# Kernel tuning notes

Hardware: AMD Instinct MI355X
Metric: run time of the kernel (lower is better)

The kernel has to match this reference:

```python
import jax, jax.numpy as jnp
import numpy as np
import math

DK = 64  # = in_dim // 4
SCALE = math.sqrt(DK)


def setup_inputs() -> dict:
    key = jax.random.key(0)
    ks = jax.random.split(key, 5)
    B, C, H, W = 8, 256, 64, 64
    x = jax.random.normal(ks[0], (B, C, H, W), dtype=jnp.float32)
    # scale weights down so pre-softmax logits are O(1)
    Wq = jax.random.normal(ks[1], (DK, C), dtype=jnp.float32) * 0.05
    Wk = jax.random.normal(ks[2], (DK, C), dtype=jnp.float32) * 0.05
    Wv = jax.random.normal(ks[3], (C, C), dtype=jnp.float32) * 0.05
    bq = jnp.zeros((DK,), dtype=jnp.float32)
    bk = jnp.zeros((DK,), dtype=jnp.float32)
    bv = jnp.zeros((C,), dtype=jnp.float32)
    gamma = jax.random.normal(ks[4], (1,), dtype=jnp.float32)
    return {"x": x, "Wq": Wq, "bq": bq, "Wk": Wk, "bk": bk,
            "Wv": Wv, "bv": bv, "gamma": gamma}


def reference(x, Wq, bq, Wk, bk, Wv, bv, gamma):
    B, C, H, W = x.shape
    N = H * W
    xf = x.reshape(B, C, N)                                   # [B,C,N]
    # 1x1 convs == per-position linear maps
    q = jnp.einsum('dc,bcn->bnd', Wq, xf) + bq                # [B,N,dk]
    k = jnp.einsum('dc,bcn->bdn', Wk, xf) + bk[:, None]       # [B,dk,N]
    v = jnp.einsum('ec,bcn->ben', Wv, xf) + bv[:, None]       # [B,C,N]
    S = jnp.einsum('bnd,bdm->bnm', q, k) / SCALE              # [B,N,N]
    attn = jax.nn.softmax(S, axis=-1)                         # softmax over keys m
    # torch: bmm(v, attn^T) -> o[b,c,m] = sum_n v[b,c,n] * attn[b,m,n]
    o = jnp.einsum('bcn,bmn->bcm', v, attn).reshape(B, C, H, W)
    return x + gamma[0] * o
```

## Files before the change

### kernel.cpp

```cpp
#include <hip/hip_runtime.h>


typedef __attribute__((ext_vector_type(8)))  short short8;
typedef __attribute__((ext_vector_type(4)))  short short4v;
typedef __attribute__((ext_vector_type(16))) float f32x16;
typedef __attribute__((ext_vector_type(4)))  float f32x4;

#define B_   8
#define C_   256
#define N_   4096
#define DK_  64
#define QSCL 0.18033688011112043f

#if defined(__has_builtin)
#if __has_builtin(__builtin_amdgcn_exp2f)
#define EXP2F(x) __builtin_amdgcn_exp2f(x)
#else
#define EXP2F(x) exp2f(x)
#endif
#else
#define EXP2F(x) exp2f(x)
#endif

__device__ __forceinline__ unsigned short bfb(float f) {
  unsigned u = __builtin_bit_cast(unsigned, f);
  unsigned r = (u + 0x7fffu + ((u >> 16) & 1u)) >> 16;
  return (unsigned short)r;
}

__device__ __forceinline__ unsigned cvtpk(float a, float b) {
  unsigned r;
  asm("v_cvt_pk_bf16_f32 %0, %1, %2" : "=v"(r) : "v"(a), "v"(b));
  return r;
}

__global__ void prep_kernel(const float* __restrict__ Wq, const float* __restrict__ bq,
                            const float* __restrict__ Wk, const float* __restrict__ bk,
                            const float* __restrict__ Wv, const float* __restrict__ bv,
                            unsigned short* __restrict__ Wc, float* __restrict__ biasc) {
  int idx = blockIdx.x * 256 + threadIdx.x;
  if (idx < 384 * 256) {
    int ch = idx >> 8, c = idx & 255;
    float v;
    if (ch < 64)       v = Wq[ch * 256 + c] * QSCL;
    else if (ch < 128) v = Wk[(ch - 64) * 256 + c];
    else               v = Wv[(ch - 128) * 256 + c];
    Wc[idx] = bfb(v);
  }
  if (idx < 384) {
    float bb;
    if (idx < 64)       bb = bq[idx] * QSCL;
    else if (idx < 128) bb = bk[idx - 64];
    else                bb = bv[idx - 128];
    biasc[idx] = bb;
  }
}

__global__ __launch_bounds__(256, 2) void proj_kernel(
    const float* __restrict__ x, const unsigned short* __restrict__ Wc,
    const float* __restrict__ biasc, unsigned short* __restrict__ Qt,
    unsigned short* __restrict__ Kt, unsigned short* __restrict__ V) {
  __shared__ unsigned short XT[64 * 256];
  const int tid = threadIdx.x;
  const int b = blockIdx.y;
  const int n0 = blockIdx.x * 64;

  {
    const f32x4* x4 = (const f32x4*)(x + ((size_t)b * C_) * N_ + n0);
    int c = tid >> 4;
    const int nl = (tid & 15) << 2;
#pragma unroll
    for (int p = 0; p < 16; ++p, c += 16) {
      f32x4 v = x4[(size_t)c * (N_ / 4) + (nl >> 2)];
#pragma unroll
      for (int i = 0; i < 4; ++i) {
        int n = nl + i;
        XT[n * 256 + ((((c >> 3) ^ (n & 15)) << 3) | (c & 7))] = bfb(v[i]);
      }
    }
  }
  __syncthreads();

  const int lane = tid & 63, li = lane & 31, hi = lane >> 5;
  const int w = tid >> 6;
  const int ch0 = 96 * w;

  f32x16 acc[2][3];
#pragma unroll
  for (int mt = 0; mt < 2; ++mt)
#pragma unroll
    for (int j = 0; j < 3; ++j)
#pragma unroll
      for (int r = 0; r < 16; ++r) acc[mt][j][r] = 0.f;

  const short8* Wc8 = (const short8*)Wc;
#pragma unroll
  for (int ks = 0; ks < 16; ++ks) {
    int chunk = 2 * ks + hi;
    short8 a0 = *(const short8*)&XT[(li) * 256 + ((chunk ^ (li & 15)) << 3)];
    short8 a1 = *(const short8*)&XT[(32 + li) * 256 + ((chunk ^ (li & 15)) << 3)];
#pragma unroll
    for (int j = 0; j < 3; ++j) {
      short8 bf = Wc8[(size_t)(ch0 + 32 * j + li) * 32 + chunk];
      acc[0][j] = __builtin_amdgcn_mfma_f32_32x32x16_bf16(a0, bf, acc[0][j], 0, 0, 0);
      acc[1][j] = __builtin_amdgcn_mfma_f32_32x32x16_bf16(a1, bf, acc[1][j], 0, 0, 0);
    }
  }

#pragma unroll
  for (int j = 0; j < 3; ++j) {
    const int chb = ch0 + 32 * j;
    const int ch = chb + li;
    const float bias = biasc[ch];
#pragma unroll
    for (int mt = 0; mt < 2; ++mt) {
      if (chb < 64) {
#pragma unroll
        for (int r = 0; r < 16; ++r) {
          int n = n0 + 32 * mt + (r & 3) + 8 * (r >> 2) + 4 * hi;
          Qt[((size_t)(b * N_ + n) << 6) + ch] = bfb(acc[mt][j][r] + bias);
        }
      } else if (chb < 128) {
#pragma unroll
        for (int r = 0; r < 16; ++r) {
          int n = n0 + 32 * mt + (r & 3) + 8 * (r >> 2) + 4 * hi;
          Kt[((size_t)(b * N_ + n) << 6) + (ch - 64)] = bfb(acc[mt][j][r] + bias);
        }
      } else {
        const int cv = ch - 128;
#pragma unroll
        for (int q = 0; q < 4; ++q) {
          short4v pk;
#pragma unroll
          for (int i = 0; i < 4; ++i) pk[i] = (short)bfb(acc[mt][j][4 * q + i] + bias);
          int n = n0 + 32 * mt + 8 * q + 4 * hi;
          *(short4v*)&V[(size_t)(b * C_ + cv) * N_ + n] = pk;
        }
      }
    }
  }
}

#define PVMFMA(PF0, PF1, PF2, PF3, VF0, VF1, VF2, VF3)                         \
  do {                                                                         \
    __builtin_amdgcn_s_setprio(1);                                             \
    acc16[0][0] = __builtin_amdgcn_mfma_f32_16x16x32_bf16(PF0, VF0, acc16[0][0], 0, 0, 0); \
    acc16[1][0] = __builtin_amdgcn_mfma_f32_16x16x32_bf16(PF1, VF0, acc16[1][0], 0, 0, 0); \
    acc16[2][0] = __builtin_amdgcn_mfma_f32_16x16x32_bf16(PF2, VF0, acc16[2][0], 0, 0, 0); \
    acc16[3][0] = __builtin_amdgcn_mfma_f32_16x16x32_bf16(PF3, VF0, acc16[3][0], 0, 0, 0); \
    acc16[0][1] = __builtin_amdgcn_mfma_f32_16x16x32_bf16(PF0, VF1, acc16[0][1], 0, 0, 0); \
    acc16[1][1] = __builtin_amdgcn_mfma_f32_16x16x32_bf16(PF1, VF1, acc16[1][1], 0, 0, 0); \
    acc16[2][1] = __builtin_amdgcn_mfma_f32_16x16x32_bf16(PF2, VF1, acc16[2][1], 0, 0, 0); \
    acc16[3][1] = __builtin_amdgcn_mfma_f32_16x16x32_bf16(PF3, VF1, acc16[3][1], 0, 0, 0); \
    acc16[0][2] = __builtin_amdgcn_mfma_f32_16x16x32_bf16(PF0, VF2, acc16[0][2], 0, 0, 0); \
    acc16[1][2] = __builtin_amdgcn_mfma_f32_16x16x32_bf16(PF1, VF2, acc16[1][2], 0, 0, 0); \
    acc16[2][2] = __builtin_amdgcn_mfma_f32_16x16x32_bf16(PF2, VF2, acc16[2][2], 0, 0, 0); \
    acc16[3][2] = __builtin_amdgcn_mfma_f32_16x16x32_bf16(PF3, VF2, acc16[3][2], 0, 0, 0); \
    acc16[0][3] = __builtin_amdgcn_mfma_f32_16x16x32_bf16(PF0, VF3, acc16[0][3], 0, 0, 0); \
    acc16[1][3] = __builtin_amdgcn_mfma_f32_16x16x32_bf16(PF1, VF3, acc16[1][3], 0, 0, 0); \
    acc16[2][3] = __builtin_amdgcn_mfma_f32_16x16x32_bf16(PF2, VF3, acc16[2][3], 0, 0, 0); \
    acc16[3][3] = __builtin_amdgcn_mfma_f32_16x16x32_bf16(PF3, VF3, acc16[3][3], 0, 0, 0); \
    __builtin_amdgcn_s_setprio(0);                                             \
  } while (0)

#define FITER(KC0, KC1, KN0, KN1, PB, VB, VN, TN)                              \
  {                                                                            \
    _Pragma("unroll") for (int mt = 0; mt < 4; ++mt) {                         \
      f32x4 st = {0.f, 0.f, 0.f, 0.f};                                         \
      st = __builtin_amdgcn_mfma_f32_16x16x32_bf16(KC0, qb[mt][0], st, 0, 0, 0); \
      st = __builtin_amdgcn_mfma_f32_16x16x32_bf16(KC1, qb[mt][1], st, 0, 0, 0); \
      float e0 = EXP2F(st[0]), e1 = EXP2F(st[1]);                              \
      float e2 = EXP2F(st[2]), e3 = EXP2F(st[3]);                              \
      den[mt] += (e0 + e1) + (e2 + e3);                                        \
      unsigned lo_ = cvtpk(e0, e1), hh_ = cvtpk(e2, e3);                       \
      unsigned long long vv_ =                                                 \
          (unsigned long long)lo_ | ((unsigned long long)hh_ << 32);           \
      *(unsigned long long*)((PB) + 2048 * mt + prow_base + pwoff) = vv_;      \
    }                                                                          \
    __syncthreads();                          \
    KN0 = *(const short8*)(Kp + (size_t)(TN) * 8192);                          \
    KN1 = *(const short8*)(Kp + (size_t)(TN) * 8192 + 64);                     \
    asm volatile("" ::: "memory");      \
    _Pragma("unroll") for (int j = 0; j < 8; ++j)                              \
      __builtin_amdgcn_global_load_lds(                                        \
          (const __attribute__((address_space(1))) unsigned int*)(srcp[j] +    \
                                                                  (size_t)(TN) * 128), \
          (__attribute__((address_space(3))) unsigned int*)((VN) + w * 8192 +  \
                                                            j * 1024),         \
          16, 0, 0);                                                           \
    {                                                                          \
      const char* vwb_ = (VB) + w * 8192 + prow_base;                          \
      const char* pb_ = (PB) + prow_base;                                      \
      short8 pf0 = *(const short8*)(pb_ + off2_0);                             \
      short8 pf1 = *(const short8*)(pb_ + 2048 + off2_0);                      \
      short8 pf2 = *(const short8*)(pb_ + 4096 + off2_0);                      \
      short8 pf3 = *(const short8*)(pb_ + 6144 + off2_0);                      \
      short8 vf0 = *(const short8*)(vwb_ + off2_0);                            \
      short8 vf1 = *(const short8*)(vwb_ + 2048 + off2_0);                     \
      short8 vf2 = *(const short8*)(vwb_ + 4096 + off2_0);                     \
      short8 vf3 = *(const short8*)(vwb_ + 6144 + off2_0);                     \
      PVMFMA(pf0, pf1, pf2, pf3, vf0, vf1, vf2, vf3);                          \
      pf0 = *(const short8*)(pb_ + off2_1);                                    \
      pf1 = *(const short8*)(pb_ + 2048 + off2_1);                             \
      pf2 = *(const short8*)(pb_ + 4096 + off2_1);                             \
      pf3 = *(const short8*)(pb_ + 6144 + off2_1);                             \
      vf0 = *(const short8*)(vwb_ + off2_1);                                   \
      vf1 = *(const short8*)(vwb_ + 2048 + off2_1);                            \
      vf2 = *(const short8*)(vwb_ + 4096 + off2_1);                            \
      vf3 = *(const short8*)(vwb_ + 6144 + off2_1);                            \
      PVMFMA(pf0, pf1, pf2, pf3, vf0, vf1, vf2, vf3);                          \
    }                                                                          \
  }

__global__ __launch_bounds__(256, 2) void flash_kernel(
    const unsigned short* __restrict__ Qt, const unsigned short* __restrict__ Kt,
    const unsigned short* __restrict__ V, const float* __restrict__ x,
    const float* __restrict__ gamma, float* __restrict__ out) {
  __shared__ char SMEM[81920];
  char* VT0 = SMEM;
  char* VT1 = SMEM + 32768;
  char* PT0 = SMEM + 65536;
  char* PT1 = SMEM + 73728;

  const int tid = threadIdx.x;
  const int lane = tid & 63;
  const int lc = lane & 15, lg = lane >> 4;
  const int w = tid >> 6;
  const int id = blockIdx.x;
  const int b = id & 7;
  const int m0 = (id >> 3) << 6;

  short8 qb[4][2];
#pragma unroll
  for (int mt = 0; mt < 4; ++mt)
#pragma unroll
    for (int ks = 0; ks < 2; ++ks)
      qb[mt][ks] = *(const short8*)(Qt + ((size_t)b * N_ + m0 + 16 * mt + lc) * 64 +
                                    32 * ks + 8 * lg);

  f32x4 acc16[4][4];
#pragma unroll
  for (int t16 = 0; t16 < 4; ++t16)
#pragma unroll
    for (int ct = 0; ct < 4; ++ct)
#pragma unroll
      for (int r = 0; r < 4; ++r) acc16[t16][ct][r] = 0.f;
  float den[4] = {0.f, 0.f, 0.f, 0.f};

  const char* Kp = (const char*)Kt + ((size_t)b * N_ + 16 * w + lc) * 128 + 16 * lg;

  const char* vsb = (const char*)V + (size_t)b * C_ * (N_ * 2);
  const char* srcp[8];
#pragma unroll
  for (int j = 0; j < 8; ++j) {
    int L = w * 8192 + j * 1024 + lane * 16;
    int rp = L >> 8, off = L & 255;
    int h = ((off >> 7) ^ (rp >> 2)) & 1;
    int c = 2 * rp + h;
    int kvb = (off ^ ((c & 15) << 4)) & 127;
    srcp[j] = vsb + (size_t)c * (N_ * 2) + kvb;
  }

  const int pkey = lc << 4;
  const int off2_0 = ((((lc & 1) << 7) | (16 * lg))) ^ pkey;
  const int off2_1 = ((((lc & 1) << 7) | 64 | (16 * lg))) ^ pkey;
  const int pwoff = ((((lc & 1) << 7) | (32 * w) | (8 * lg))) ^ pkey;
  const int prow_base = (lc >> 1) * 256;

  short8 kfA0, kfA1, kfB0, kfB1;
  kfA0 = *(const short8*)(Kp);
  kfA1 = *(const short8*)(Kp + 64);
  asm volatile("" ::: "memory");
#pragma unroll
  for (int j = 0; j < 8; ++j)
    __builtin_amdgcn_global_load_lds(
        (const __attribute__((address_space(1))) unsigned int*)(srcp[j]),
        (__attribute__((address_space(3))) unsigned int*)(VT0 + w * 8192 + j * 1024),
        16, 0, 0);

  for (int t = 0; t < 64; t += 2) {
    const int tn1 = t + 1;
    FITER(kfA0, kfA1, kfB0, kfB1, PT0, VT0, VT1, tn1);
    const int tn2 = (t + 2) & 63;
    FITER(kfB0, kfB1, kfA0, kfA1, PT1, VT1, VT0, tn2);
  }

  float* den_lds = (float*)PT0;
#pragma unroll
  for (int mt = 0; mt < 4; ++mt) {
    float d = den[mt];
    d += __shfl_xor(d, 16);
    d += __shfl_xor(d, 32);
    if (lg == 0) den_lds[w * 64 + mt * 16 + lc] = d;
  }
  __syncthreads();

  const float g = gamma[0];
  float ig[4];
#pragma unroll
  for (int mt = 0; mt < 4; ++mt) {
    float dtot = den_lds[0 * 64 + mt * 16 + lc] + den_lds[1 * 64 + mt * 16 + lc] +
                 den_lds[2 * 64 + mt * 16 + lc] + den_lds[3 * 64 + mt * 16 + lc];
    ig[mt] = g / dtot;
  }

#pragma unroll
  for (int t16 = 0; t16 < 4; ++t16) {
    f32x4 idn;
#pragma unroll
    for (int r = 0; r < 4; ++r)
      idn[r] = __shfl(ig[t16], 4 * lg + r);
#pragma unroll
    for (int ct = 0; ct < 4; ++ct) {
      size_t off = ((size_t)b * C_ + 64 * w + 16 * ct + lc) * N_ + m0 + 16 * t16 + 4 * lg;
      f32x4 xv = *(const f32x4*)(x + off);
      f32x4 o;
#pragma unroll
      for (int r = 0; r < 4; ++r) o[r] = xv[r] + idn[r] * acc16[t16][ct][r];
      *(f32x4*)(out + off) = o;
    }
  }
}

extern "C" void kernel_launch(void* const* d_in, const int* in_sizes, int n_in,
                              void* d_out, int out_size, void* d_ws, size_t ws_size,
                              hipStream_t stream) {
  const float* x = (const float*)d_in[0];
  const float* Wq = (const float*)d_in[1];
  const float* bq = (const float*)d_in[2];
  const float* Wk = (const float*)d_in[3];
  const float* bk = (const float*)d_in[4];
  const float* Wv = (const float*)d_in[5];
  const float* bv = (const float*)d_in[6];
  const float* gamma = (const float*)d_in[7];
  float* out = (float*)d_out;

  char* ws = (char*)d_ws;
  unsigned short* Wc = (unsigned short*)(ws);
  float* biasc = (float*)(ws + 196608);
  unsigned short* Qt = (unsigned short*)(ws + 198144);
  unsigned short* Kt = (unsigned short*)(ws + 198144 + 4194304);
  unsigned short* Vv = (unsigned short*)(ws + 198144 + 8388608);

  prep_kernel<<<384, 256, 0, stream>>>(Wq, bq, Wk, bk, Wv, bv, Wc, biasc);
  proj_kernel<<<dim3(64, 8), 256, 0, stream>>>(x, Wc, biasc, Qt, Kt, Vv);
  flash_kernel<<<512, 256, 0, stream>>>(Qt, Kt, Vv, x, gamma, out);
}
```

Before: 136.7 us.

## Software-pipeline QK^T/exp of next tile with PV MFMA of current tile

Restructures the main loop so that each phase computes the scores and exponentials for tile t+1 into the alternate P buffer while issuing the P·V MFMAs for tile t, with one barrier per phase instead of a barrier between the score and PV stages. A prologue computes the first tile's P and K fragments are prefetched two tiles ahead. The aim is to overlap exp/VALU work and LDS stores with matrix-core work and hide barrier latency, at the cost of higher register pressure from holding both fragment sets and more complex buffer indexing.

```diff
diff --git a/kernel.cpp b/kernel.cpp
--- a/kernel.cpp
+++ b/kernel.cpp
@@ -163,53 +163,52 @@
     __builtin_amdgcn_s_setprio(0);                                             \
   } while (0)
 
-#define FITER(KC0, KC1, KN0, KN1, PB, VB, VN, TN)                              \
+#define S_BODY(KS0, KS1, PBW)                                                  \
+  _Pragma("unroll") for (int mt = 0; mt < 4; ++mt) {                           \
+    f32x4 st = {0.f, 0.f, 0.f, 0.f};                                           \
+    st = __builtin_amdgcn_mfma_f32_16x16x32_bf16(KS0, qb[mt][0], st, 0, 0, 0); \
+    st = __builtin_amdgcn_mfma_f32_16x16x32_bf16(KS1, qb[mt][1], st, 0, 0, 0); \
+    float e0 = EXP2F(st[0]), e1 = EXP2F(st[1]);                                \
+    float e2 = EXP2F(st[2]), e3 = EXP2F(st[3]);                                \
+    den[mt] += (e0 + e1) + (e2 + e3);                                          \
+    unsigned lo_ = cvtpk(e0, e1), hh_ = cvtpk(e2, e3);                         \
+    unsigned long long vv_ =                                                   \
+        (unsigned long long)lo_ | ((unsigned long long)hh_ << 32);             \
+    *(unsigned long long*)((PBW) + 2048 * mt + prow_base + pwoff) = vv_;       \
+  }
+
+#define MPHASE(PBR, PBW, VBR, VBW, KS0, KS1, KL0, KL1, TDMA, TK, DO_S)         \
   {                                                                            \
-    _Pragma("unroll") for (int mt = 0; mt < 4; ++mt) {                         \
-      f32x4 st = {0.f, 0.f, 0.f, 0.f};                                         \
-      st = __builtin_amdgcn_mfma_f32_16x16x32_bf16(KC0, qb[mt][0], st, 0, 0, 0); \
-      st = __builtin_amdgcn_mfma_f32_16x16x32_bf16(KC1, qb[mt][1], st, 0, 0, 0); \
-      float e0 = EXP2F(st[0]), e1 = EXP2F(st[1]);                              \
-      float e2 = EXP2F(st[2]), e3 = EXP2F(st[3]);                              \
-      den[mt] += (e0 + e1) + (e2 + e3);                                        \
-      unsigned lo_ = cvtpk(e0, e1), hh_ = cvtpk(e2, e3);                       \
-      unsigned long long vv_ =                                                 \
-          (unsigned long long)lo_ | ((unsigned long long)hh_ << 32);           \
-      *(unsigned long long*)((PB) + 2048 * mt + prow_base + pwoff) = vv_;      \
-    }                                                                          \
-    __syncthreads();                          \
-    KN0 = *(const short8*)(Kp + (size_t)(TN) * 8192);                          \
-    KN1 = *(const short8*)(Kp + (size_t)(TN) * 8192 + 64);                     \
-    asm volatile("" ::: "memory");      \
     _Pragma("unroll") for (int j = 0; j < 8; ++j)                              \
       __builtin_amdgcn_global_load_lds(                                        \
           (const __attribute__((address_space(1))) unsigned int*)(srcp[j] +    \
-                                                                  (size_t)(TN) * 128), \
-          (__attribute__((address_space(3))) unsigned int*)((VN) + w * 8192 +  \
-                                                            j * 1024),         \
-          16, 0, 0);                                                           \
-    {                                                                          \
-      const char* vwb_ = (VB) + w * 8192 + prow_base;                          \
-      const char* pb_ = (PB) + prow_base;                                      \
-      short8 pf0 = *(const short8*)(pb_ + off2_0);                             \
-      short8 pf1 = *(const short8*)(pb_ + 2048 + off2_0);                      \
-      short8 pf2 = *(const short8*)(pb_ + 4096 + off2_0);                      \
-      short8 pf3 = *(const short8*)(pb_ + 6144 + off2_0);                      \
-      short8 vf0 = *(const short8*)(vwb_ + off2_0);                            \
-      short8 vf1 = *(const short8*)(vwb_ + 2048 + off2_0);                     \
-      short8 vf2 = *(const short8*)(vwb_ + 4096 + off2_0);                     \
-      short8 vf3 = *(const short8*)(vwb_ + 6144 + off2_0);                     \
-      PVMFMA(pf0, pf1, pf2, pf3, vf0, vf1, vf2, vf3);                          \
-      pf0 = *(const short8*)(pb_ + off2_1);                                    \
-      pf1 = *(const short8*)(pb_ + 2048 + off2_1);                             \
-      pf2 = *(const short8*)(pb_ + 4096 + off2_1);                             \
-      pf3 = *(const short8*)(pb_ + 6144 + off2_1);                             \
-      vf0 = *(const short8*)(vwb_ + off2_1);                                   \
-      vf1 = *(const short8*)(vwb_ + 2048 + off2_1);                            \
-      vf2 = *(const short8*)(vwb_ + 4096 + off2_1);                            \
-      vf3 = *(const short8*)(vwb_ + 6144 + off2_1);                            \
-      PVMFMA(pf0, pf1, pf2, pf3, vf0, vf1, vf2, vf3);                          \
-    }                                                                          \
+              (size_t)((TDMA) & 63) * 128),                                    \
+          (__attribute__((address_space(3))) unsigned int*)((VBW) + w * 8192 + \
+              j * 1024), 16, 0, 0);                                            \
+    KL0 = *(const short8*)(Kp + (size_t)((TK) & 63) * 8192);                   \
+    KL1 = *(const short8*)(Kp + (size_t)((TK) & 63) * 8192 + 64);              \
+    const char* vwb_ = (VBR) + w * 8192 + prow_base;                           \
+    const char* pb_ = (PBR) + prow_base;                                       \
+    short8 pf0 = *(const short8*)(pb_ + off2_0);                               \
+    short8 pf1 = *(const short8*)(pb_ + 2048 + off2_0);                        \
+    short8 pf2 = *(const short8*)(pb_ + 4096 + off2_0);                        \
+    short8 pf3 = *(const short8*)(pb_ + 6144 + off2_0);                        \
+    short8 vf0 = *(const short8*)(vwb_ + off2_0);                              \
+    short8 vf1 = *(const short8*)(vwb_ + 2048 + off2_0);                       \
+    short8 vf2 = *(const short8*)(vwb_ + 4096 + off2_0);                       \
+    short8 vf3 = *(const short8*)(vwb_ + 6144 + off2_0);                       \
+    if (DO_S) { S_BODY(KS0, KS1, PBW) }                                        \
+    short8 pg0 = *(const short8*)(pb_ + off2_1);                               \
+    short8 pg1 = *(const short8*)(pb_ + 2048 + off2_1);                        \
+    short8 pg2 = *(const short8*)(pb_ + 4096 + off2_1);                        \
+    short8 pg3 = *(const short8*)(pb_ + 6144 + off2_1);                        \
+    short8 vg0 = *(const short8*)(vwb_ + off2_1);                              \
+    short8 vg1 = *(const short8*)(vwb_ + 2048 + off2_1);                       \
+    short8 vg2 = *(const short8*)(vwb_ + 4096 + off2_1);                       \
+    short8 vg3 = *(const short8*)(vwb_ + 6144 + off2_1);                       \
+    PVMFMA(pf0, pf1, pf2, pf3, vf0, vf1, vf2, vf3);                            \
+    PVMFMA(pg0, pg1, pg2, pg3, vg0, vg1, vg2, vg3);                            \
+    __syncthreads();                                                           \
   }
 
 __global__ __launch_bounds__(256, 2) void flash_kernel(
@@ -267,22 +266,26 @@
   const int pwoff = ((((lc & 1) << 7) | (32 * w) | (8 * lg))) ^ pkey;
   const int prow_base = (lc >> 1) * 256;
 
-  short8 kfA0, kfA1, kfB0, kfB1;
-  kfA0 = *(const short8*)(Kp);
-  kfA1 = *(const short8*)(Kp + 64);
-  asm volatile("" ::: "memory");
-#pragma unroll
-  for (int j = 0; j < 8; ++j)
-    __builtin_amdgcn_global_load_lds(
-        (const __attribute__((address_space(1))) unsigned int*)(srcp[j]),
-        (__attribute__((address_space(3))) unsigned int*)(VT0 + w * 8192 + j * 1024),
-        16, 0, 0);
+  short8 kA0, kA1, kB0, kB1;
+  {
+    short8 k00 = *(const short8*)(Kp);
+    short8 k01 = *(const short8*)(Kp + 64);
+    kA0 = *(const short8*)(Kp + 8192);
+    kA1 = *(const short8*)(Kp + 8192 + 64);
+#pragma unroll
+    for (int j = 0; j < 8; ++j)
+      __builtin_amdgcn_global_load_lds(
+          (const __attribute__((address_space(1))) unsigned int*)(srcp[j]),
+          (__attribute__((address_space(3))) unsigned int*)(VT0 + w * 8192 + j * 1024),
+          16, 0, 0);
+    __syncthreads();
+    S_BODY(k00, k01, PT0)
+    __syncthreads();
+  }
 
   for (int t = 0; t < 64; t += 2) {
-    const int tn1 = t + 1;
-    FITER(kfA0, kfA1, kfB0, kfB1, PT0, VT0, VT1, tn1);
-    const int tn2 = (t + 2) & 63;
-    FITER(kfB0, kfB1, kfA0, kfA1, PT1, VT1, VT0, tn2);
+    MPHASE(PT0, PT1, VT0, VT1, kA0, kA1, kB0, kB1, t + 1, t + 2, 1);
+    MPHASE(PT1, PT0, VT1, VT0, kB0, kB1, kA0, kA1, t + 2, t + 3, (t + 1) < 63);
   }
 
   float* den_lds = (float*)PT0;
```

Result: slower. 144.7 us (+5.8%).
